# Optimization experiments

Hardware: AMD Instinct MI355X
Metric: run time of the kernel (lower is better)

Reference implementation:

```python
import jax, jax.numpy as jnp
import numpy as np

N = 50000      # nodes
E = 800000     # edges (avg degree 16)
F_IN = 128     # input feature dim
HID = 128      # 2 * out_classes
OUT = 64       # out_classes


def setup_inputs() -> dict:
    key = jax.random.key(0)
    ks = jax.random.split(key, 12)
    x = jax.random.normal(ks[0], (N, F_IN), jnp.float32)
    edge_index = jax.random.randint(ks[1], (2, E), 0, N, jnp.int32)
    def lin(k, fi, fo):
        return jax.random.normal(k, (fi, fo), jnp.float32) / np.float32(np.sqrt(fi))
    return {
        "x": x,
        "edge_index": edge_index,
        "W1": lin(ks[2], F_IN, HID), "b1": jnp.zeros((HID,), jnp.float32),
        "W2": lin(ks[3], HID, HID),  "b2": jnp.zeros((HID,), jnp.float32),
        "W3": lin(ks[4], HID, HID),  "b3": jnp.zeros((HID,), jnp.float32),
        "jk_w": jax.random.normal(ks[5], (3,), jnp.float32),
        "fc_W": lin(ks[6], HID, OUT), "fc_b": jnp.zeros((OUT,), jnp.float32),
    }


def _gcn_conv(h, W, b, row, col, n):
    """PyG GCNConv: linear -> add self-loops -> sym-normalized aggregate -> bias."""
    h = h @ W                                        # [n, d_out]
    loops = jnp.arange(n, dtype=row.dtype)
    r = jnp.concatenate([row, loops])                # sources
    c = jnp.concatenate([col, loops])                # targets
    deg = jax.ops.segment_sum(jnp.ones_like(c, h.dtype), c, num_segments=n)
    dinv = jnp.where(deg > 0, jax.lax.rsqrt(deg), 0.0)
    norm = dinv[r] * dinv[c]                         # [E+n]
    msg = h[r] * norm[:, None]                       # gather + scale
    return jax.ops.segment_sum(msg, c, num_segments=n) + b


def _neighbor_mean(h, row, col, n):
    """sample_neighbors with scale_factor=2: exact mean over out-neighbors,
    own feature when degree == 0 (top-k branch is provably dead code)."""
    s = jax.ops.segment_sum(h[col], row, num_segments=n)
    deg = jax.ops.segment_sum(jnp.ones_like(row, h.dtype), row, num_segments=n)
    mean = s / jnp.maximum(deg, 1.0)[:, None]
    return jnp.where((deg > 0)[:, None], mean, h)


def reference(x, edge_index, W1, b1, W2, b2, W3, b3, jk_w, fc_W, fc_b):
    row, col = edge_index[0], edge_index[1]
    n = x.shape[0]
    # layer 0: GCN -> ReLU -> (dropout: eval identity) -> neighbor sampling
    h0 = jax.nn.relu(_gcn_conv(x, W1, b1, row, col, n))
    h0 = _neighbor_mean(h0, row, col, n)
    # layer 1: GCN -> ReLU; historical-activation update is identity on first call
    h1 = jax.nn.relu(_gcn_conv(h0, W2, b2, row, col, n))
    # layer 2
    h2 = jax.nn.relu(_gcn_conv(h1, W3, b3, row, col, n))
    # dynamic JK aggregation
    w = jax.nn.softmax(jk_w)
    h = w[0] * h0 + w[1] * h1 + w[2] * h2
    return h @ fc_W + fc_b
```

## Files before the change

### kernel.cpp

```cpp
#include <hip/hip_runtime.h>
#include <stdint.h>

typedef unsigned int  uint32;
typedef unsigned short u16;

typedef short bfx8 __attribute__((ext_vector_type(8)));
typedef float f32x4 __attribute__((ext_vector_type(4)));
typedef float f32x2 __attribute__((ext_vector_type(2)));

#define NBP 256
#define CH  2048
#define BS  4608

__device__ __forceinline__ float b2f(u16 u) {
    union { uint32 i; float f; } v; v.i = ((uint32)u) << 16; return v.f;
}
__device__ __forceinline__ u16 f2b(float f) {
    union { float f; uint32 i; } v; v.f = f;
    uint32 u = v.i;
    return (u16)((u + 0x7fffu + ((u >> 16) & 1u)) >> 16);
}
__device__ __forceinline__ float blo(uint32 u) {
    union { uint32 i; float f; } v; v.i = u << 16; return v.f;
}
__device__ __forceinline__ float bhi(uint32 u) {
    union { uint32 i; float f; } v; v.i = u & 0xffff0000u; return v.f;
}
__device__ __forceinline__ uint32 packbf(float a, float b) {
    return (uint32)f2b(a) | ((uint32)f2b(b) << 16);
}
__device__ __forceinline__ void splitf(float x, u16& h, u16& l) {
    h = f2b(x);
    l = f2b(x - b2f(h));
}
__device__ __forceinline__ void split8(const float* __restrict__ p, bfx8& hi, bfx8& lo) {
    f32x4 a = *(const f32x4*)p;
    f32x4 b = *(const f32x4*)(p + 4);
    float x[8] = {a[0], a[1], a[2], a[3], b[0], b[1], b[2], b[3]};
#pragma unroll
    for (int j = 0; j < 8; ++j) {
        u16 h, l; splitf(x[j], h, l);
        hi[j] = (short)h; lo[j] = (short)l;
    }
}

__global__ __launch_bounds__(256) void k_init(
    int* __restrict__ curC, int* __restrict__ curR,
    const float* __restrict__ W1, const float* __restrict__ W2,
    const float* __restrict__ W3, const float* __restrict__ fcW,
    u16* __restrict__ WTh, u16* __restrict__ WTl, int WTN) {
    int t = threadIdx.x;
    if (blockIdx.x == 0) {
        curC[t] = t * BS;
        curR[t] = t * BS;
        return;
    }
    int i = ((int)blockIdx.x - 1) * 256 + t;
    if (i >= WTN) return;
    float w;
    if (i < 3 * 16384) {
        int m = i >> 14, j = i & 16383;
        int fo = j >> 7, fi = j & 127;
        const float* W = (m == 0) ? W1 : (m == 1) ? W2 : W3;
        w = W[fi * 128 + fo];
    } else {
        int j = i - 3 * 16384;
        int fo = j >> 7, fi = j & 127;
        w = fcW[fi * 64 + fo];
    }
    u16 h, l; splitf(w, h, l);
    WTh[i] = h; WTl[i] = l;
}

__global__ __launch_bounds__(256) void k_gemm0(
    const float* __restrict__ A, const u16* __restrict__ WTh, const u16* __restrict__ WTl,
    u16* __restrict__ G, int M) {
    const int lane = threadIdx.x & 63;
    const int q = lane >> 4, l = lane & 15;
    int rbase = blockIdx.x * 128 + (threadIdx.x >> 6) * 32;
    if (rbase >= M) return;
    int r0 = rbase + l;      if (r0 >= M) r0 = M - 1;
    int r1 = rbase + 16 + l; if (r1 >= M) r1 = M - 1;

    f32x4 acc[2][8];
#pragma unroll
    for (int i = 0; i < 2; ++i)
#pragma unroll
        for (int j = 0; j < 8; ++j) acc[i][j] = (f32x4){0.f, 0.f, 0.f, 0.f};

#pragma unroll
    for (int kc = 0; kc < 4; ++kc) {
        int k0 = kc * 32 + q * 8;
        bfx8 ah0, al0, ah1, al1;
        split8(A + (size_t)r0 * 128 + k0, ah0, al0);
        split8(A + (size_t)r1 * 128 + k0, ah1, al1);
#pragma unroll
        for (int ct = 0; ct < 8; ++ct) {
            bfx8 bh = *(const bfx8*)(WTh + (ct * 16 + l) * 128 + k0);
            bfx8 bl = *(const bfx8*)(WTl + (ct * 16 + l) * 128 + k0);
            acc[0][ct] = __builtin_amdgcn_mfma_f32_16x16x32_bf16(ah0, bh, acc[0][ct], 0, 0, 0);
            acc[0][ct] = __builtin_amdgcn_mfma_f32_16x16x32_bf16(ah0, bl, acc[0][ct], 0, 0, 0);
            acc[0][ct] = __builtin_amdgcn_mfma_f32_16x16x32_bf16(al0, bh, acc[0][ct], 0, 0, 0);
            acc[1][ct] = __builtin_amdgcn_mfma_f32_16x16x32_bf16(ah1, bh, acc[1][ct], 0, 0, 0);
            acc[1][ct] = __builtin_amdgcn_mfma_f32_16x16x32_bf16(ah1, bl, acc[1][ct], 0, 0, 0);
            acc[1][ct] = __builtin_amdgcn_mfma_f32_16x16x32_bf16(al1, bh, acc[1][ct], 0, 0, 0);
        }
    }
#pragma unroll
    for (int rs = 0; rs < 2; ++rs) {
#pragma unroll
        for (int rr = 0; rr < 4; ++rr) {
            int rw = rbase + rs * 16 + q * 4 + rr;
            if (rw < M) {
#pragma unroll
                for (int ct = 0; ct < 8; ++ct)
                    G[(size_t)rw * 128 + ct * 16 + l] = f2b(acc[rs][ct][rr]);
            }
        }
    }
}

__global__ __launch_bounds__(256) void k_gemm1p(
    const u16* __restrict__ Ah,
    const u16* __restrict__ WTh, const u16* __restrict__ WTl,
    const float* __restrict__ dinv, u16* __restrict__ G, int M) {
    const int lane = threadIdx.x & 63;
    const int q = lane >> 4, l = lane & 15;
    int rbase = blockIdx.x * 128 + (threadIdx.x >> 6) * 32;
    if (rbase >= M) return;
    int r0 = rbase + l;      if (r0 >= M) r0 = M - 1;
    int r1 = rbase + 16 + l; if (r1 >= M) r1 = M - 1;

    f32x4 acc[2][8];
#pragma unroll
    for (int i = 0; i < 2; ++i)
#pragma unroll
        for (int j = 0; j < 8; ++j) acc[i][j] = (f32x4){0.f, 0.f, 0.f, 0.f};

#pragma unroll
    for (int kc = 0; kc < 4; ++kc) {
        int k0 = kc * 32 + q * 8;
        bfx8 ah0 = *(const bfx8*)(Ah + (size_t)r0 * 128 + k0);
        bfx8 ah1 = *(const bfx8*)(Ah + (size_t)r1 * 128 + k0);
#pragma unroll
        for (int ct = 0; ct < 8; ++ct) {
            bfx8 bh = *(const bfx8*)(WTh + (ct * 16 + l) * 128 + k0);
            bfx8 bl = *(const bfx8*)(WTl + (ct * 16 + l) * 128 + k0);
            acc[0][ct] = __builtin_amdgcn_mfma_f32_16x16x32_bf16(ah0, bh, acc[0][ct], 0, 0, 0);
            acc[0][ct] = __builtin_amdgcn_mfma_f32_16x16x32_bf16(ah0, bl, acc[0][ct], 0, 0, 0);
            acc[1][ct] = __builtin_amdgcn_mfma_f32_16x16x32_bf16(ah1, bh, acc[1][ct], 0, 0, 0);
            acc[1][ct] = __builtin_amdgcn_mfma_f32_16x16x32_bf16(ah1, bl, acc[1][ct], 0, 0, 0);
        }
    }
#pragma unroll
    for (int rs = 0; rs < 2; ++rs) {
#pragma unroll
        for (int rr = 0; rr < 4; ++rr) {
            int rw = rbase + rs * 16 + q * 4 + rr;
            if (rw < M) {
                float dv = dinv[rw];
#pragma unroll
                for (int ct = 0; ct < 8; ++ct)
                    G[(size_t)rw * 128 + ct * 16 + l] = f2b(acc[rs][ct][rr] * dv);
            }
        }
    }
}

__global__ __launch_bounds__(256) void k_partC(
    const int* __restrict__ row, const int* __restrict__ col, int E,
    int* __restrict__ curC, int* __restrict__ curR,
    uint32* __restrict__ partC, uint32* __restrict__ partR) {
    __shared__ uint32 stagedC[CH], stagedR[CH];
    __shared__ int hp[NBP], expk[NBP], curp[NBP], runC[NBP], runR[NBP];
    __shared__ int wsum[4];
    int t = threadIdx.x;
    int lane = t & 63, wid = t >> 6;
    int base = blockIdx.x * CH;
    int n = E - base; if (n > CH) n = CH;

    int er[8], ec[8];
#pragma unroll
    for (int j = 0; j < 8; ++j) {
        int i = t + j * 256;
        if (i < n) { er[j] = row[base + i]; ec[j] = col[base + i]; }
        else er[j] = -1;
    }
    hp[t] = 0;
    __syncthreads();
#pragma unroll
    for (int j = 0; j < 8; ++j) {
        if (er[j] >= 0) {
            atomicAdd(&hp[ec[j] >> 8], 1);
            atomicAdd(&hp[er[j] >> 8], 0x10000);
        }
    }
    __syncthreads();
    int v = hp[t];
    int x = v;
#pragma unroll
    for (int d = 1; d < 64; d <<= 1) {
        int u = __shfl_up(x, d);
        if (lane >= d) x += u;
    }
    if (lane == 63) wsum[wid] = x;
    __syncthreads();
    int add = 0;
    for (int i = 0; i < wid; ++i) add += wsum[i];
    int ex = x + add - v;
    expk[t] = ex;
    curp[t] = ex;
    int vC = v & 0xffff, vR = v >> 16;
    runC[t] = vC ? atomicAdd(&curC[t], vC) : 0;
    runR[t] = vR ? atomicAdd(&curR[t], vR) : 0;
    __syncthreads();
#pragma unroll
    for (int j = 0; j < 8; ++j) {
        if (er[j] >= 0) {
            int cb = ec[j] >> 8, rb = er[j] >> 8;
            int pC = atomicAdd(&curp[cb], 1) & 0xffff;
            stagedC[pC] = ((uint32)ec[j] << 16) | (uint32)er[j];
            int pR = atomicAdd(&curp[rb], 0x10000) >> 16;
            stagedR[pR] = ((uint32)er[j] << 16) | (uint32)ec[j];
        }
    }
    __syncthreads();
    for (int i = t; i < n; i += 256) {
        uint32 pv = stagedC[i];
        int b = pv >> 24;
        partC[runC[b] + (i - (expk[b] & 0xffff))] = pv;
    }
    for (int i = t; i < n; i += 256) {
        uint32 pv = stagedR[i];
        int b = pv >> 24;
        partR[runR[b] + (i - (expk[b] >> 16))] = pv;
    }
}

__global__ __launch_bounds__(256) void k_fillD(
    const uint32* __restrict__ partC, const uint32* __restrict__ partR,
    const int* __restrict__ curC, const int* __restrict__ curR,
    int* __restrict__ off_in, int* __restrict__ end_in,
    int* __restrict__ off_out, int* __restrict__ end_out,
    u16* __restrict__ csr_src, u16* __restrict__ csr_dst,
    float* __restrict__ dinv, int NB, int N) {
    int part = ((int)blockIdx.x >= NB) ? 1 : 0;
    int b = (int)blockIdx.x - part * NB;
    const uint32* arr = part ? partR : partC;
    const int* curA   = part ? curR : curC;
    int* offA         = part ? off_out : off_in;
    int* endA         = part ? end_out : end_in;
    u16* csr          = part ? csr_dst : csr_src;
    int t = threadIdx.x;
    int lane = t & 63, wid = t >> 6;
    int base = b * BS, end = curA[b];
    __shared__ int cnt[NBP], cur[NBP];
    __shared__ int wsum[4];
    cnt[t] = 0;
    __syncthreads();
    for (int i = base + t; i < end; i += 256)
        atomicAdd(&cnt[(arr[i] >> 16) & 255], 1);
    __syncthreads();
    int v = cnt[t];
    int x = v;
#pragma unroll
    for (int d = 1; d < 64; d <<= 1) {
        int u = __shfl_up(x, d);
        if (lane >= d) x += u;
    }
    if (lane == 63) wsum[wid] = x;
    __syncthreads();
    int add = 0;
    for (int i = 0; i < wid; ++i) add += wsum[i];
    int ex = x + add - v;
    cur[t] = ex;
    int node = (b << 8) + t;
    if (node < N) {
        offA[node] = base + ex;
        endA[node] = base + ex + v;
        if (part == 0) dinv[node] = rsqrtf((float)(v + 1));
    }
    __syncthreads();
    for (int i = base + t; i < end; i += 256) {
        uint32 pv = arr[i];
        int local = (pv >> 16) & 255;
        int pos = atomicAdd(&cur[local], 1);
        csr[base + pos] = (u16)(pv & 0xffffu);
    }
}

template <int MODE>
__global__ __launch_bounds__(256) void k_agg(
    const uint32* __restrict__ g, const u16* __restrict__ csr_src,
    const int* __restrict__ off, const int* __restrict__ endo,
    const float* __restrict__ dinv,
    const f32x2* __restrict__ bias, uint32* __restrict__ outH, int n) {
    int w = (blockIdx.x * 256 + threadIdx.x) >> 6;
    if (w >= n) return;
    int lane = threadIdx.x & 63;
    float dc = dinv[w];
    uint32 sv = g[(size_t)w * 64 + lane];
    float s0, s1;
    if (MODE == 0) { s0 = blo(sv) * dc; s1 = bhi(sv) * dc; }
    else           { s0 = blo(sv);      s1 = bhi(sv); }
    int e = off[w], e1 = endo[w];
    for (; e + 16 <= e1; e += 16) {
        int ix[16];
#pragma unroll
        for (int j = 0; j < 16; ++j) ix[j] = csr_src[e + j];
        uint32 vv[16];
#pragma unroll
        for (int j = 0; j < 16; ++j) vv[j] = g[(size_t)ix[j] * 64 + lane];
        if (MODE == 0) {
            float dm[16];
#pragma unroll
            for (int j = 0; j < 16; ++j) dm[j] = dinv[ix[j]];
#pragma unroll
            for (int j = 0; j < 16; ++j) {
                s0 = fmaf(blo(vv[j]), dm[j], s0);
                s1 = fmaf(bhi(vv[j]), dm[j], s1);
            }
        } else {
#pragma unroll
            for (int j = 0; j < 16; ++j) { s0 += blo(vv[j]); s1 += bhi(vv[j]); }
        }
    }
    for (; e + 4 <= e1; e += 4) {
        int ix[4];
#pragma unroll
        for (int j = 0; j < 4; ++j) ix[j] = csr_src[e + j];
        uint32 vv[4];
#pragma unroll
        for (int j = 0; j < 4; ++j) vv[j] = g[(size_t)ix[j] * 64 + lane];
        if (MODE == 0) {
            float dm[4];
#pragma unroll
            for (int j = 0; j < 4; ++j) dm[j] = dinv[ix[j]];
#pragma unroll
            for (int j = 0; j < 4; ++j) {
                s0 = fmaf(blo(vv[j]), dm[j], s0);
                s1 = fmaf(bhi(vv[j]), dm[j], s1);
            }
        } else {
#pragma unroll
            for (int j = 0; j < 4; ++j) { s0 += blo(vv[j]); s1 += bhi(vv[j]); }
        }
    }
    for (; e < e1; ++e) {
        int ix = csr_src[e];
        uint32 v = g[(size_t)ix * 64 + lane];
        if (MODE == 0) {
            float dm = dinv[ix];
            s0 = fmaf(blo(v), dm, s0);
            s1 = fmaf(bhi(v), dm, s1);
        } else {
            s0 += blo(v); s1 += bhi(v);
        }
    }
    f32x2 bb = bias[lane];
    float o0 = fmaxf(fmaf(s0, dc, bb[0]), 0.f);
    float o1 = fmaxf(fmaf(s1, dc, bb[1]), 0.f);
    outH[(size_t)w * 64 + lane] = packbf(o0, o1);
}

__global__ __launch_bounds__(256) void k_mean(
    const uint32* __restrict__ h, const u16* __restrict__ csr_dst,
    const int* __restrict__ off, const int* __restrict__ endo,
    uint32* __restrict__ outH, int n) {
    int w = (blockIdx.x * 256 + threadIdx.x) >> 6;
    if (w >= n) return;
    int lane = threadIdx.x & 63;
    int e = off[w], e1 = endo[w];
    int d = e1 - e;
    float s0 = 0.f, s1 = 0.f;
    for (; e + 16 <= e1; e += 16) {
        int ix[16];
#pragma unroll
        for (int j = 0; j < 16; ++j) ix[j] = csr_dst[e + j];
        uint32 vv[16];
#pragma unroll
        for (int j = 0; j < 16; ++j) vv[j] = h[(size_t)ix[j] * 64 + lane];
#pragma unroll
        for (int j = 0; j < 16; ++j) { s0 += blo(vv[j]); s1 += bhi(vv[j]); }
    }
    for (; e + 4 <= e1; e += 4) {
        int ix[4];
#pragma unroll
        for (int j = 0; j < 4; ++j) ix[j] = csr_dst[e + j];
        uint32 vv[4];
#pragma unroll
        for (int j = 0; j < 4; ++j) vv[j] = h[(size_t)ix[j] * 64 + lane];
#pragma unroll
        for (int j = 0; j < 4; ++j) { s0 += blo(vv[j]); s1 += bhi(vv[j]); }
    }
    for (; e < e1; ++e) {
        uint32 v = h[(size_t)csr_dst[e] * 64 + lane];
        s0 += blo(v); s1 += bhi(v);
    }
    float o0, o1;
    if (d > 0) {
        float inv = 1.f / (float)d;
        o0 = s0 * inv; o1 = s1 * inv;
    } else {
        uint32 sv = h[(size_t)w * 64 + lane];
        o0 = blo(sv); o1 = bhi(sv);
    }
    outH[(size_t)w * 64 + lane] = packbf(o0, o1);
}

__global__ __launch_bounds__(256) void k_final(
    const u16* __restrict__ h0, const u16* __restrict__ h1,
    const u16* __restrict__ h2, const float* __restrict__ jkw,
    const u16* __restrict__ fcWTh, const u16* __restrict__ fcWTl,
    const float* __restrict__ fcb, float* __restrict__ out, int M) {
    float a0 = jkw[0], a1 = jkw[1], a2 = jkw[2];
    float mx = fmaxf(a0, fmaxf(a1, a2));
    float e0 = expf(a0 - mx), e1 = expf(a1 - mx), e2 = expf(a2 - mx);
    float inv = 1.f / (e0 + e1 + e2);
    float w0 = e0 * inv, w1 = e1 * inv, w2 = e2 * inv;

    const int lane = threadIdx.x & 63;
    const int q = lane >> 4, l = lane & 15;
    int rbase = blockIdx.x * 128 + (threadIdx.x >> 6) * 32;
    if (rbase >= M) return;
    int r0 = rbase + l;      if (r0 >= M) r0 = M - 1;
    int r1 = rbase + 16 + l; if (r1 >= M) r1 = M - 1;

    f32x4 acc[2][4];
#pragma unroll
    for (int i = 0; i < 2; ++i)
#pragma unroll
        for (int j = 0; j < 4; ++j) acc[i][j] = (f32x4){0.f, 0.f, 0.f, 0.f};

    union U8 { bfx8 v; u16 u[8]; };

#pragma unroll
    for (int kc = 0; kc < 4; ++kc) {
        int k0 = kc * 32 + q * 8;
        bfx8 ah[2];
        const int rr2[2] = {r0, r1};
#pragma unroll
        for (int half = 0; half < 2; ++half) {
            size_t o = (size_t)rr2[half] * 128 + k0;
            U8 x0, x1, x2, rh;
            x0.v = *(const bfx8*)(h0 + o);
            x1.v = *(const bfx8*)(h1 + o);
            x2.v = *(const bfx8*)(h2 + o);
#pragma unroll
            for (int j = 0; j < 8; ++j) {
                float c = w0 * b2f(x0.u[j]) + w1 * b2f(x1.u[j]) + w2 * b2f(x2.u[j]);
                rh.u[j] = f2b(c);
            }
            ah[half] = rh.v;
        }
#pragma unroll
        for (int ct = 0; ct < 4; ++ct) {
            bfx8 bh = *(const bfx8*)(fcWTh + (ct * 16 + l) * 128 + k0);
            bfx8 bl = *(const bfx8*)(fcWTl + (ct * 16 + l) * 128 + k0);
#pragma unroll
            for (int half = 0; half < 2; ++half) {
                acc[half][ct] = __builtin_amdgcn_mfma_f32_16x16x32_bf16(ah[half], bh, acc[half][ct], 0, 0, 0);
                acc[half][ct] = __builtin_amdgcn_mfma_f32_16x16x32_bf16(ah[half], bl, acc[half][ct], 0, 0, 0);
            }
        }
    }
#pragma unroll
    for (int rs = 0; rs < 2; ++rs) {
#pragma unroll
        for (int rr = 0; rr < 4; ++rr) {
            int rw = rbase + rs * 16 + q * 4 + rr;
            if (rw < M) {
#pragma unroll
                for (int ct = 0; ct < 4; ++ct) {
                    int cc = ct * 16 + l;
                    out[(size_t)rw * 64 + cc] = acc[rs][ct][rr] + fcb[cc];
                }
            }
        }
    }
}

extern "C" void kernel_launch(void* const* d_in, const int* in_sizes, int n_in,
                              void* d_out, int out_size, void* d_ws, size_t ws_size,
                              hipStream_t stream) {
    const int N = in_sizes[0] / 128;
    const int E = in_sizes[1] / 2;
    const int NB = (N + 255) >> 8;

    const float* x    = (const float*)d_in[0];
    const int* row    = (const int*)d_in[1];
    const int* col    = row + E;
    const float* W1   = (const float*)d_in[2];
    const float* b1   = (const float*)d_in[3];
    const float* W2   = (const float*)d_in[4];
    const float* b2   = (const float*)d_in[5];
    const float* W3   = (const float*)d_in[6];
    const float* b3   = (const float*)d_in[7];
    const float* jkw  = (const float*)d_in[8];
    const float* fcW  = (const float*)d_in[9];
    const float* fcb  = (const float*)d_in[10];
    float* outp       = (float*)d_out;

    char* ws = (char*)d_ws;
    size_t off = 0;
    auto alloc = [&](size_t bytes) -> char* {
        char* p = ws + off;
        off += (bytes + 255) & ~(size_t)255;
        return p;
    };
    int* curC   = (int*)alloc((size_t)NBP * sizeof(int));
    int* curR   = (int*)alloc((size_t)NBP * sizeof(int));
    int* off_in  = (int*)alloc((size_t)N * sizeof(int));
    int* end_in  = (int*)alloc((size_t)N * sizeof(int));
    int* off_out = (int*)alloc((size_t)N * sizeof(int));
    int* end_out = (int*)alloc((size_t)N * sizeof(int));
    uint32* partC = (uint32*)alloc((size_t)NBP * BS * sizeof(uint32));
    uint32* partR = (uint32*)alloc((size_t)NBP * BS * sizeof(uint32));
    u16* csr_src = (u16*)alloc((size_t)NBP * BS * sizeof(u16));
    u16* csr_dst = (u16*)alloc((size_t)NBP * BS * sizeof(u16));
    float* dinv  = (float*)alloc((size_t)N * sizeof(float));
    const int WTN = 3 * 16384 + 8192;
    u16* WTh = (u16*)alloc((size_t)WTN * sizeof(u16));
    u16* WTl = (u16*)alloc((size_t)WTN * sizeof(u16));
    size_t FB = (size_t)N * 128 * sizeof(u16);
    u16* gbuf = (u16*)alloc(FB);
    u16* t0   = (u16*)alloc(FB);
    u16* h0   = (u16*)alloc(FB);
    u16* h1   = (u16*)alloc(FB);
    u16* h2   = (u16*)alloc(FB);

    const int B = 256;
    int Gh = (E + CH - 1) / CH;
    int Gg = (N + 127) / 128;
    int Gwt = (WTN + B - 1) / B;

    k_init<<<1 + Gwt, B, 0, stream>>>(curC, curR, W1, W2, W3, fcW, WTh, WTl, WTN);
    k_gemm0<<<Gg, B, 0, stream>>>(x, WTh, WTl, gbuf, N);
    k_partC<<<Gh, B, 0, stream>>>(row, col, E, curC, curR, partC, partR);
    k_fillD<<<2 * NB, B, 0, stream>>>(partC, partR, curC, curR,
                                      off_in, end_in, off_out, end_out,
                                      csr_src, csr_dst, dinv, NB, N);

    int aggG = (N + 3) / 4;

    k_agg<0><<<aggG, B, 0, stream>>>((const uint32*)gbuf, csr_src, off_in, end_in, dinv,
                                     (const f32x2*)b1, (uint32*)t0, N);
    k_mean<<<aggG, B, 0, stream>>>((const uint32*)t0, csr_dst, off_out, end_out,
                                   (uint32*)h0, N);
    k_gemm1p<<<Gg, B, 0, stream>>>(h0, WTh + 16384, WTl + 16384, dinv, gbuf, N);
    k_agg<1><<<aggG, B, 0, stream>>>((const uint32*)gbuf, csr_src, off_in, end_in, dinv,
                                     (const f32x2*)b2, (uint32*)h1, N);
    k_gemm1p<<<Gg, B, 0, stream>>>(h1, WTh + 2 * 16384, WTl + 2 * 16384, dinv, gbuf, N);
    k_agg<1><<<aggG, B, 0, stream>>>((const uint32*)gbuf, csr_src, off_in, end_in, dinv,
                                     (const f32x2*)b3, (uint32*)h2, N);
    k_final<<<Gg, B, 0, stream>>>(h0, h1, h2, jkw,
                                  WTh + 3 * 16384, WTl + 3 * 16384, fcb, outp, N);
}
```

Measured before the change: 340.1 us.

## Split edges across half-waves with 8-byte gathers, prescale layer-0 GEMM by dinv

Aggregation and mean kernels now have each half of a wavefront handle alternate edges and load 8-byte (4 bf16) chunks per lane, combining the halves with a cross-half shuffle. This halves the loads per edge and doubles the memory-level parallelism of the irregular gathers. The first GEMM now runs after CSR/degree construction so it can pre-multiply rows by dinv, which removes the per-neighbour dinv gather from the layer-0 aggregation. It also drops the low-part split of x, leaving the x operand of that GEMM in single bf16, which loses some precision.

```diff
diff --git a/kernel.cpp b/kernel.cpp
--- a/kernel.cpp
+++ b/kernel.cpp
@@ -32,16 +32,6 @@
 __device__ __forceinline__ void splitf(float x, u16& h, u16& l) {
     h = f2b(x);
     l = f2b(x - b2f(h));
-}
-__device__ __forceinline__ void split8(const float* __restrict__ p, bfx8& hi, bfx8& lo) {
-    f32x4 a = *(const f32x4*)p;
-    f32x4 b = *(const f32x4*)(p + 4);
-    float x[8] = {a[0], a[1], a[2], a[3], b[0], b[1], b[2], b[3]};
-#pragma unroll
-    for (int j = 0; j < 8; ++j) {
-        u16 h, l; splitf(x[j], h, l);
-        hi[j] = (short)h; lo[j] = (short)l;
-    }
 }
 
 __global__ __launch_bounds__(256) void k_init(
@@ -70,101 +60,6 @@
     }
     u16 h, l; splitf(w, h, l);
     WTh[i] = h; WTl[i] = l;
-}
-
-__global__ __launch_bounds__(256) void k_gemm0(
-    const float* __restrict__ A, const u16* __restrict__ WTh, const u16* __restrict__ WTl,
-    u16* __restrict__ G, int M) {
-    const int lane = threadIdx.x & 63;
-    const int q = lane >> 4, l = lane & 15;
-    int rbase = blockIdx.x * 128 + (threadIdx.x >> 6) * 32;
-    if (rbase >= M) return;
-    int r0 = rbase + l;      if (r0 >= M) r0 = M - 1;
-    int r1 = rbase + 16 + l; if (r1 >= M) r1 = M - 1;
-
-    f32x4 acc[2][8];
-#pragma unroll
-    for (int i = 0; i < 2; ++i)
-#pragma unroll
-        for (int j = 0; j < 8; ++j) acc[i][j] = (f32x4){0.f, 0.f, 0.f, 0.f};
-
-#pragma unroll
-    for (int kc = 0; kc < 4; ++kc) {
-        int k0 = kc * 32 + q * 8;
-        bfx8 ah0, al0, ah1, al1;
-        split8(A + (size_t)r0 * 128 + k0, ah0, al0);
-        split8(A + (size_t)r1 * 128 + k0, ah1, al1);
-#pragma unroll
-        for (int ct = 0; ct < 8; ++ct) {
-            bfx8 bh = *(const bfx8*)(WTh + (ct * 16 + l) * 128 + k0);
-            bfx8 bl = *(const bfx8*)(WTl + (ct * 16 + l) * 128 + k0);
-            acc[0][ct] = __builtin_amdgcn_mfma_f32_16x16x32_bf16(ah0, bh, acc[0][ct], 0, 0, 0);
-            acc[0][ct] = __builtin_amdgcn_mfma_f32_16x16x32_bf16(ah0, bl, acc[0][ct], 0, 0, 0);
-            acc[0][ct] = __builtin_amdgcn_mfma_f32_16x16x32_bf16(al0, bh, acc[0][ct], 0, 0, 0);
-            acc[1][ct] = __builtin_amdgcn_mfma_f32_16x16x32_bf16(ah1, bh, acc[1][ct], 0, 0, 0);
-            acc[1][ct] = __builtin_amdgcn_mfma_f32_16x16x32_bf16(ah1, bl, acc[1][ct], 0, 0, 0);
-            acc[1][ct] = __builtin_amdgcn_mfma_f32_16x16x32_bf16(al1, bh, acc[1][ct], 0, 0, 0);
-        }
-    }
-#pragma unroll
-    for (int rs = 0; rs < 2; ++rs) {
-#pragma unroll
-        for (int rr = 0; rr < 4; ++rr) {
-            int rw = rbase + rs * 16 + q * 4 + rr;
-            if (rw < M) {
-#pragma unroll
-                for (int ct = 0; ct < 8; ++ct)
-                    G[(size_t)rw * 128 + ct * 16 + l] = f2b(acc[rs][ct][rr]);
-            }
-        }
-    }
-}
-
-__global__ __launch_bounds__(256) void k_gemm1p(
-    const u16* __restrict__ Ah,
-    const u16* __restrict__ WTh, const u16* __restrict__ WTl,
-    const float* __restrict__ dinv, u16* __restrict__ G, int M) {
-    const int lane = threadIdx.x & 63;
-    const int q = lane >> 4, l = lane & 15;
-    int rbase = blockIdx.x * 128 + (threadIdx.x >> 6) * 32;
-    if (rbase >= M) return;
-    int r0 = rbase + l;      if (r0 >= M) r0 = M - 1;
-    int r1 = rbase + 16 + l; if (r1 >= M) r1 = M - 1;
-
-    f32x4 acc[2][8];
-#pragma unroll
-    for (int i = 0; i < 2; ++i)
-#pragma unroll
-        for (int j = 0; j < 8; ++j) acc[i][j] = (f32x4){0.f, 0.f, 0.f, 0.f};
-
-#pragma unroll
-    for (int kc = 0; kc < 4; ++kc) {
-        int k0 = kc * 32 + q * 8;
-        bfx8 ah0 = *(const bfx8*)(Ah + (size_t)r0 * 128 + k0);
-        bfx8 ah1 = *(const bfx8*)(Ah + (size_t)r1 * 128 + k0);
-#pragma unroll
-        for (int ct = 0; ct < 8; ++ct) {
-            bfx8 bh = *(const bfx8*)(WTh + (ct * 16 + l) * 128 + k0);
-            bfx8 bl = *(const bfx8*)(WTl + (ct * 16 + l) * 128 + k0);
-            acc[0][ct] = __builtin_amdgcn_mfma_f32_16x16x32_bf16(ah0, bh, acc[0][ct], 0, 0, 0);
-            acc[0][ct] = __builtin_amdgcn_mfma_f32_16x16x32_bf16(ah0, bl, acc[0][ct], 0, 0, 0);
-            acc[1][ct] = __builtin_amdgcn_mfma_f32_16x16x32_bf16(ah1, bh, acc[1][ct], 0, 0, 0);
-            acc[1][ct] = __builtin_amdgcn_mfma_f32_16x16x32_bf16(ah1, bl, acc[1][ct], 0, 0, 0);
-        }
-    }
-#pragma unroll
-    for (int rs = 0; rs < 2; ++rs) {
-#pragma unroll
-        for (int rr = 0; rr < 4; ++rr) {
-            int rw = rbase + rs * 16 + q * 4 + rr;
-            if (rw < M) {
-                float dv = dinv[rw];
-#pragma unroll
-                for (int ct = 0; ct < 8; ++ct)
-                    G[(size_t)rw * 128 + ct * 16 + l] = f2b(acc[rs][ct][rr] * dv);
-            }
-        }
-    }
 }
 
 __global__ __launch_bounds__(256) void k_partC(
@@ -289,123 +184,226 @@
     }
 }
 
-template <int MODE>
+__global__ __launch_bounds__(256) void k_gemm0(
+    const float* __restrict__ A, const u16* __restrict__ WTh, const u16* __restrict__ WTl,
+    const float* __restrict__ dinv, u16* __restrict__ G, int M) {
+    const int lane = threadIdx.x & 63;
+    const int q = lane >> 4, l = lane & 15;
+    int rbase = blockIdx.x * 128 + (threadIdx.x >> 6) * 32;
+    if (rbase >= M) return;
+    int r0 = rbase + l;      if (r0 >= M) r0 = M - 1;
+    int r1 = rbase + 16 + l; if (r1 >= M) r1 = M - 1;
+
+    f32x4 acc[2][8];
+#pragma unroll
+    for (int i = 0; i < 2; ++i)
+#pragma unroll
+        for (int j = 0; j < 8; ++j) acc[i][j] = (f32x4){0.f, 0.f, 0.f, 0.f};
+
+#pragma unroll
+    for (int kc = 0; kc < 4; ++kc) {
+        int k0 = kc * 32 + q * 8;
+        bfx8 ah0, ah1;
+        {
+            f32x4 a = *(const f32x4*)(A + (size_t)r0 * 128 + k0);
+            f32x4 b = *(const f32x4*)(A + (size_t)r0 * 128 + k0 + 4);
+            float xx[8] = {a[0], a[1], a[2], a[3], b[0], b[1], b[2], b[3]};
+#pragma unroll
+            for (int j = 0; j < 8; ++j) ah0[j] = (short)f2b(xx[j]);
+        }
+        {
+            f32x4 a = *(const f32x4*)(A + (size_t)r1 * 128 + k0);
+            f32x4 b = *(const f32x4*)(A + (size_t)r1 * 128 + k0 + 4);
+            float xx[8] = {a[0], a[1], a[2], a[3], b[0], b[1], b[2], b[3]};
+#pragma unroll
+            for (int j = 0; j < 8; ++j) ah1[j] = (short)f2b(xx[j]);
+        }
+#pragma unroll
+        for (int ct = 0; ct < 8; ++ct) {
+            bfx8 bh = *(const bfx8*)(WTh + (ct * 16 + l) * 128 + k0);
+            bfx8 bl = *(const bfx8*)(WTl + (ct * 16 + l) * 128 + k0);
+            acc[0][ct] = __builtin_amdgcn_mfma_f32_16x16x32_bf16(ah0, bh, acc[0][ct], 0, 0, 0);
+            acc[0][ct] = __builtin_amdgcn_mfma_f32_16x16x32_bf16(ah0, bl, acc[0][ct], 0, 0, 0);
+            acc[1][ct] = __builtin_amdgcn_mfma_f32_16x16x32_bf16(ah1, bh, acc[1][ct], 0, 0, 0);
+            acc[1][ct] = __builtin_amdgcn_mfma_f32_16x16x32_bf16(ah1, bl, acc[1][ct], 0, 0, 0);
+        }
+    }
+#pragma unroll
+    for (int rs = 0; rs < 2; ++rs) {
+#pragma unroll
+        for (int rr = 0; rr < 4; ++rr) {
+            int rw = rbase + rs * 16 + q * 4 + rr;
+            if (rw < M) {
+                float dv = dinv[rw];
+#pragma unroll
+                for (int ct = 0; ct < 8; ++ct)
+                    G[(size_t)rw * 128 + ct * 16 + l] = f2b(acc[rs][ct][rr] * dv);
+            }
+        }
+    }
+}
+
+__global__ __launch_bounds__(256) void k_gemm1p(
+    const u16* __restrict__ Ah,
+    const u16* __restrict__ WTh, const u16* __restrict__ WTl,
+    const float* __restrict__ dinv, u16* __restrict__ G, int M) {
+    const int lane = threadIdx.x & 63;
+    const int q = lane >> 4, l = lane & 15;
+    int rbase = blockIdx.x * 128 + (threadIdx.x >> 6) * 32;
+    if (rbase >= M) return;
+    int r0 = rbase + l;      if (r0 >= M) r0 = M - 1;
+    int r1 = rbase + 16 + l; if (r1 >= M) r1 = M - 1;
+
+    f32x4 acc[2][8];
+#pragma unroll
+    for (int i = 0; i < 2; ++i)
+#pragma unroll
+        for (int j = 0; j < 8; ++j) acc[i][j] = (f32x4){0.f, 0.f, 0.f, 0.f};
+
+#pragma unroll
+    for (int kc = 0; kc < 4; ++kc) {
+        int k0 = kc * 32 + q * 8;
+        bfx8 ah0 = *(const bfx8*)(Ah + (size_t)r0 * 128 + k0);
+        bfx8 ah1 = *(const bfx8*)(Ah + (size_t)r1 * 128 + k0);
+#pragma unroll
+        for (int ct = 0; ct < 8; ++ct) {
+            bfx8 bh = *(const bfx8*)(WTh + (ct * 16 + l) * 128 + k0);
+            bfx8 bl = *(const bfx8*)(WTl + (ct * 16 + l) * 128 + k0);
+            acc[0][ct] = __builtin_amdgcn_mfma_f32_16x16x32_bf16(ah0, bh, acc[0][ct], 0, 0, 0);
+            acc[0][ct] = __builtin_amdgcn_mfma_f32_16x16x32_bf16(ah0, bl, acc[0][ct], 0, 0, 0);
+            acc[1][ct] = __builtin_amdgcn_mfma_f32_16x16x32_bf16(ah1, bh, acc[1][ct], 0, 0, 0);
+            acc[1][ct] = __builtin_amdgcn_mfma_f32_16x16x32_bf16(ah1, bl, acc[1][ct], 0, 0, 0);
+        }
+    }
+#pragma unroll
+    for (int rs = 0; rs < 2; ++rs) {
+#pragma unroll
+        for (int rr = 0; rr < 4; ++rr) {
+            int rw = rbase + rs * 16 + q * 4 + rr;
+            if (rw < M) {
+                float dv = dinv[rw];
+#pragma unroll
+                for (int ct = 0; ct < 8; ++ct)
+                    G[(size_t)rw * 128 + ct * 16 + l] = f2b(acc[rs][ct][rr] * dv);
+            }
+        }
+    }
+}
+
 __global__ __launch_bounds__(256) void k_agg(
-    const uint32* __restrict__ g, const u16* __restrict__ csr_src,
+    const uint2* __restrict__ g2, const u16* __restrict__ csr,
     const int* __restrict__ off, const int* __restrict__ endo,
-    const float* __restrict__ dinv,
-    const f32x2* __restrict__ bias, uint32* __restrict__ outH, int n) {
+    const float* __restrict__ dinv, const f32x4* __restrict__ bias4,
+    uint2* __restrict__ outH, int n) {
     int w = (blockIdx.x * 256 + threadIdx.x) >> 6;
     if (w >= n) return;
     int lane = threadIdx.x & 63;
+    int half = lane >> 5, sl = lane & 31;
+    uint2 sv = g2[(size_t)w * 32 + sl];
+    float s0, s1, s2, s3;
+    if (half == 0) { s0 = blo(sv.x); s1 = bhi(sv.x); s2 = blo(sv.y); s3 = bhi(sv.y); }
+    else           { s0 = s1 = s2 = s3 = 0.f; }
+    int e = off[w], e1 = endo[w];
+    int deg = e1 - e;
+    int pairs = deg >> 1;
+    int p = 0;
+    for (; p + 8 <= pairs; p += 8) {
+        int ix[8];
+#pragma unroll
+        for (int j = 0; j < 8; ++j) ix[j] = csr[e + 2 * (p + j) + half];
+        uint2 vv[8];
+#pragma unroll
+        for (int j = 0; j < 8; ++j) vv[j] = g2[(size_t)ix[j] * 32 + sl];
+#pragma unroll
+        for (int j = 0; j < 8; ++j) {
+            s0 += blo(vv[j].x); s1 += bhi(vv[j].x);
+            s2 += blo(vv[j].y); s3 += bhi(vv[j].y);
+        }
+    }
+    for (; p < pairs; ++p) {
+        int ix = csr[e + 2 * p + half];
+        uint2 vv = g2[(size_t)ix * 32 + sl];
+        s0 += blo(vv.x); s1 += bhi(vv.x);
+        s2 += blo(vv.y); s3 += bhi(vv.y);
+    }
+    if (deg & 1) {
+        int ix = csr[e1 - 1];
+        uint2 vv = g2[(size_t)ix * 32 + sl];
+        if (half == 0) {
+            s0 += blo(vv.x); s1 += bhi(vv.x);
+            s2 += blo(vv.y); s3 += bhi(vv.y);
+        }
+    }
+    s0 += __shfl_xor(s0, 32);
+    s1 += __shfl_xor(s1, 32);
+    s2 += __shfl_xor(s2, 32);
+    s3 += __shfl_xor(s3, 32);
+    if (half) return;
     float dc = dinv[w];
-    uint32 sv = g[(size_t)w * 64 + lane];
-    float s0, s1;
-    if (MODE == 0) { s0 = blo(sv) * dc; s1 = bhi(sv) * dc; }
-    else           { s0 = blo(sv);      s1 = bhi(sv); }
-    int e = off[w], e1 = endo[w];
-    for (; e + 16 <= e1; e += 16) {
-        int ix[16];
-#pragma unroll
-        for (int j = 0; j < 16; ++j) ix[j] = csr_src[e + j];
-        uint32 vv[16];
-#pragma unroll
-        for (int j = 0; j < 16; ++j) vv[j] = g[(size_t)ix[j] * 64 + lane];
-        if (MODE == 0) {
-            float dm[16];
-#pragma unroll
-            for (int j = 0; j < 16; ++j) dm[j] = dinv[ix[j]];
-#pragma unroll
-            for (int j = 0; j < 16; ++j) {
-                s0 = fmaf(blo(vv[j]), dm[j], s0);
-                s1 = fmaf(bhi(vv[j]), dm[j], s1);
-            }
-        } else {
-#pragma unroll
-            for (int j = 0; j < 16; ++j) { s0 += blo(vv[j]); s1 += bhi(vv[j]); }
-        }
-    }
-    for (; e + 4 <= e1; e += 4) {
-        int ix[4];
-#pragma unroll
-        for (int j = 0; j < 4; ++j) ix[j] = csr_src[e + j];
-        uint32 vv[4];
-#pragma unroll
-        for (int j = 0; j < 4; ++j) vv[j] = g[(size_t)ix[j] * 64 + lane];
-        if (MODE == 0) {
-            float dm[4];
-#pragma unroll
-            for (int j = 0; j < 4; ++j) dm[j] = dinv[ix[j]];
-#pragma unroll
-            for (int j = 0; j < 4; ++j) {
-                s0 = fmaf(blo(vv[j]), dm[j], s0);
-                s1 = fmaf(bhi(vv[j]), dm[j], s1);
-            }
-        } else {
-#pragma unroll
-            for (int j = 0; j < 4; ++j) { s0 += blo(vv[j]); s1 += bhi(vv[j]); }
-        }
-    }
-    for (; e < e1; ++e) {
-        int ix = csr_src[e];
-        uint32 v = g[(size_t)ix * 64 + lane];
-        if (MODE == 0) {
-            float dm = dinv[ix];
-            s0 = fmaf(blo(v), dm, s0);
-            s1 = fmaf(bhi(v), dm, s1);
-        } else {
-            s0 += blo(v); s1 += bhi(v);
-        }
-    }
-    f32x2 bb = bias[lane];
+    f32x4 bb = bias4[sl];
     float o0 = fmaxf(fmaf(s0, dc, bb[0]), 0.f);
     float o1 = fmaxf(fmaf(s1, dc, bb[1]), 0.f);
-    outH[(size_t)w * 64 + lane] = packbf(o0, o1);
+    float o2 = fmaxf(fmaf(s2, dc, bb[2]), 0.f);
+    float o3 = fmaxf(fmaf(s3, dc, bb[3]), 0.f);
+    uint2 o; o.x = packbf(o0, o1); o.y = packbf(o2, o3);
+    outH[(size_t)w * 32 + sl] = o;
 }
 
 __global__ __launch_bounds__(256) void k_mean(
-    const uint32* __restrict__ h, const u16* __restrict__ csr_dst,
+    const uint2* __restrict__ h2, const u16* __restrict__ csr,
     const int* __restrict__ off, const int* __restrict__ endo,
-    uint32* __restrict__ outH, int n) {
+    uint2* __restrict__ outH, int n) {
     int w = (blockIdx.x * 256 + threadIdx.x) >> 6;
     if (w >= n) return;
     int lane = threadIdx.x & 63;
+    int half = lane >> 5, sl = lane & 31;
     int e = off[w], e1 = endo[w];
-    int d = e1 - e;
-    float s0 = 0.f, s1 = 0.f;
-    for (; e + 16 <= e1; e += 16) {
-        int ix[16];
-#pragma unroll
-        for (int j = 0; j < 16; ++j) ix[j] = csr_dst[e + j];
-        uint32 vv[16];
-#pragma unroll
-        for (int j = 0; j < 16; ++j) vv[j] = h[(size_t)ix[j] * 64 + lane];
-#pragma unroll
-        for (int j = 0; j < 16; ++j) { s0 += blo(vv[j]); s1 += bhi(vv[j]); }
-    }
-    for (; e + 4 <= e1; e += 4) {
-        int ix[4];
-#pragma unroll
-        for (int j = 0; j < 4; ++j) ix[j] = csr_dst[e + j];
-        uint32 vv[4];
-#pragma unroll
-        for (int j = 0; j < 4; ++j) vv[j] = h[(size_t)ix[j] * 64 + lane];
-#pragma unroll
-        for (int j = 0; j < 4; ++j) { s0 += blo(vv[j]); s1 += bhi(vv[j]); }
-    }
-    for (; e < e1; ++e) {
-        uint32 v = h[(size_t)csr_dst[e] * 64 + lane];
-        s0 += blo(v); s1 += bhi(v);
-    }
-    float o0, o1;
-    if (d > 0) {
-        float inv = 1.f / (float)d;
-        o0 = s0 * inv; o1 = s1 * inv;
+    int deg = e1 - e;
+    float s0 = 0.f, s1 = 0.f, s2 = 0.f, s3 = 0.f;
+    int pairs = deg >> 1;
+    int p = 0;
+    for (; p + 8 <= pairs; p += 8) {
+        int ix[8];
+#pragma unroll
+        for (int j = 0; j < 8; ++j) ix[j] = csr[e + 2 * (p + j) + half];
+        uint2 vv[8];
+#pragma unroll
+        for (int j = 0; j < 8; ++j) vv[j] = h2[(size_t)ix[j] * 32 + sl];
+#pragma unroll
+        for (int j = 0; j < 8; ++j) {
+            s0 += blo(vv[j].x); s1 += bhi(vv[j].x);
+            s2 += blo(vv[j].y); s3 += bhi(vv[j].y);
+        }
+    }
+    for (; p < pairs; ++p) {
+        int ix = csr[e + 2 * p + half];
+        uint2 vv = h2[(size_t)ix * 32 + sl];
+        s0 += blo(vv.x); s1 += bhi(vv.x);
+        s2 += blo(vv.y); s3 += bhi(vv.y);
+    }
+    if (deg & 1) {
+        int ix = csr[e1 - 1];
+        uint2 vv = h2[(size_t)ix * 32 + sl];
+        if (half == 0) {
+            s0 += blo(vv.x); s1 += bhi(vv.x);
+            s2 += blo(vv.y); s3 += bhi(vv.y);
+        }
+    }
+    s0 += __shfl_xor(s0, 32);
+    s1 += __shfl_xor(s1, 32);
+    s2 += __shfl_xor(s2, 32);
+    s3 += __shfl_xor(s3, 32);
+    if (half) return;
+    float o0, o1, o2, o3;
+    if (deg > 0) {
+        float inv = 1.f / (float)deg;
+        o0 = s0 * inv; o1 = s1 * inv; o2 = s2 * inv; o3 = s3 * inv;
     } else {
-        uint32 sv = h[(size_t)w * 64 + lane];
-        o0 = blo(sv); o1 = bhi(sv);
-    }
-    outH[(size_t)w * 64 + lane] = packbf(o0, o1);
+        uint2 sv = h2[(size_t)w * 32 + sl];
+        o0 = blo(sv.x); o1 = bhi(sv.x); o2 = blo(sv.y); o3 = bhi(sv.y);
+    }
+    uint2 o; o.x = packbf(o0, o1); o.y = packbf(o2, o3);
+    outH[(size_t)w * 32 + sl] = o;
 }
 
 __global__ __launch_bounds__(256) void k_final(
@@ -535,24 +533,24 @@
     int Gwt = (WTN + B - 1) / B;
 
     k_init<<<1 + Gwt, B, 0, stream>>>(curC, curR, W1, W2, W3, fcW, WTh, WTl, WTN);
-    k_gemm0<<<Gg, B, 0, stream>>>(x, WTh, WTl, gbuf, N);
     k_partC<<<Gh, B, 0, stream>>>(row, col, E, curC, curR, partC, partR);
     k_fillD<<<2 * NB, B, 0, stream>>>(partC, partR, curC, curR,
                                       off_in, end_in, off_out, end_out,
                                       csr_src, csr_dst, dinv, NB, N);
+    k_gemm0<<<Gg, B, 0, stream>>>(x, WTh, WTl, dinv, gbuf, N);
 
     int aggG = (N + 3) / 4;
 
-    k_agg<0><<<aggG, B, 0, stream>>>((const uint32*)gbuf, csr_src, off_in, end_in, dinv,
-                                     (const f32x2*)b1, (uint32*)t0, N);
-    k_mean<<<aggG, B, 0, stream>>>((const uint32*)t0, csr_dst, off_out, end_out,
-                                   (uint32*)h0, N);
+    k_agg<<<aggG, B, 0, stream>>>((const uint2*)gbuf, csr_src, off_in, end_in, dinv,
+                                  (const f32x4*)b1, (uint2*)t0, N);
+    k_mean<<<aggG, B, 0, stream>>>((const uint2*)t0, csr_dst, off_out, end_out,
+                                   (uint2*)h0, N);
     k_gemm1p<<<Gg, B, 0, stream>>>(h0, WTh + 16384, WTl + 16384, dinv, gbuf, N);
-    k_agg<1><<<aggG, B, 0, stream>>>((const uint32*)gbuf, csr_src, off_in, end_in, dinv,
-                                     (const f32x2*)b2, (uint32*)h1, N);
+    k_agg<<<aggG, B, 0, stream>>>((const uint2*)gbuf, csr_src, off_in, end_in, dinv,
+                                  (const f32x4*)b2, (uint2*)h1, N);
     k_gemm1p<<<Gg, B, 0, stream>>>(h1, WTh + 2 * 16384, WTl + 2 * 16384, dinv, gbuf, N);
-    k_agg<1><<<aggG, B, 0, stream>>>((const uint32*)gbuf, csr_src, off_in, end_in, dinv,
-                                     (const f32x2*)b3, (uint32*)h2, N);
+    k_agg<<<aggG, B, 0, stream>>>((const uint2*)gbuf, csr_src, off_in, end_in, dinv,
+                                  (const f32x4*)b3, (uint2*)h2, N);
     k_final<<<Gg, B, 0, stream>>>(h0, h1, h2, jkw,
                                   WTh + 3 * 16384, WTl + 3 * 16384, fcb, outp, N);
 }
```

After: 362.3 us. +6.5%, slower.
